# Kernel tuning notes

Measured on AMD Instinct MI355X. Metric: run time of the kernel, lower is better.

The kernel has to match this reference:

```python
import math
import jax, jax.numpy as jnp
from jax import lax
import numpy as np

B, T, D = 4, 8192, 1024
NUM_PATCHES = 512
EPS = 1e-6

def setup_inputs() -> dict:
    key = jax.random.key(0)
    ks = jax.random.split(key, 4)
    h = D // 2
    x = jax.random.normal(ks[0], (B, T, D), dtype=jnp.float32)
    conv1_w = jax.random.normal(ks[1], (h, D, 3), dtype=jnp.float32) * 0.02
    conv1_b = jnp.zeros((h,), jnp.float32)
    conv2_w = jax.random.normal(ks[2], (1, h, 3), dtype=jnp.float32) * 0.02
    conv2_b = jnp.zeros((1,), jnp.float32)
    norm_w = jnp.ones((D,), jnp.float32)
    return {"x": x, "conv1_w": conv1_w, "conv1_b": conv1_b,
            "conv2_w": conv2_w, "conv2_b": conv2_b, "norm_w": norm_w}

def _conv1d(x_ncw, w, b):
    y = lax.conv_general_dilated(x_ncw, w, window_strides=(1,), padding=[(1, 1)],
                                 dimension_numbers=("NCW", "OIW", "NCW"))
    return y + b[None, :, None]

def reference(x, conv1_w, conv1_b, conv2_w, conv2_b, norm_w):
    b, t, d = x.shape
    k = NUM_PATCHES
    seg = t // k  # T divisible by k, so all segments have equal length

    # LearnedBoundaryPredictor: conv -> gelu -> conv -> logits (B, T)
    xc = jnp.transpose(x, (0, 2, 1))  # (B, D, T)
    hcv = jax.nn.gelu(_conv1d(xc, conv1_w, conv1_b), approximate=False)
    logits = _conv1d(hcv, conv2_w, conv2_b)[:, 0, :]  # (B, T)

    # per-segment softmax-weighted centroid + normalized entropy (vectorized)
    seg_logits = logits.reshape(b, k, seg)
    w = jax.nn.softmax(seg_logits, axis=-1)                      # (B, k, seg)
    pos = jnp.arange(t, dtype=x.dtype).reshape(1, k, seg)
    boundaries = jnp.sum(w * pos, axis=-1)                        # (B, k)
    ent = -jnp.sum(w * jnp.log(jnp.clip(w, 1e-8)), axis=-1)
    entropy_signal = ent / jnp.asarray(math.log(max(seg, 2)), x.dtype)

    # gather byte embeddings at integer boundary positions
    idx = jnp.clip(boundaries.astype(jnp.int32), 0, t - 1)       # (B, k)
    patches = jnp.take_along_axis(x, idx[:, :, None], axis=1)    # (B, k, D)

    # RMSNorm
    rms = lax.rsqrt(jnp.mean(patches * patches, axis=-1, keepdims=True) + EPS)
    out = patches * rms * norm_w
    return out, entropy_signal
```

## Files before the change

kernel.cpp:

```cpp
#include <hip/hip_runtime.h>
#include <hip/hip_bf16.h>
#include <math.h>

#define T_LEN 8192
#define D_DIM 1024
#define H_DIM 512
#define NPATCH 512
#define SEG 16

typedef _Float16 f16;
typedef _Float16 f16x4 __attribute__((ext_vector_type(4)));
typedef _Float16 f16x8 __attribute__((ext_vector_type(8)));
typedef float f32x4 __attribute__((ext_vector_type(4)));

#define BMR 256
#define BNR 128
#define NBM2 128
#define NBN2 4
#define QL2 258
#define PADT (T_LEN + 2)
#define RSCALE 2048.0f
#define RINV   4.8828125e-4f

#define BUFB 49152
#define NSTEP 96

__device__ __forceinline__ void gll16(const void* g, void* l) {
    __builtin_amdgcn_global_load_lds((const __attribute__((address_space(1))) void*)g,
                                     (__attribute__((address_space(3))) void*)l, 16, 0, 0);
}

__global__ __launch_bounds__(256) void k_split_x(const float* __restrict__ x,
                                                 f16* __restrict__ xh, f16* __restrict__ xls) {
    size_t i4 = (size_t)blockIdx.x * 256 + threadIdx.x;
    size_t e = i4 * 4;
    int d = (int)(e % D_DIM);
    size_t row = e / D_DIM;
    int pt = (int)(row % PADT);
    int b = (int)(row / PADT);
    f16x4 h, lo;
    if (pt == 0 || pt == PADT - 1) {
        h = (f16x4){0, 0, 0, 0}; lo = (f16x4){0, 0, 0, 0};
    } else {
        float4 v = *(const float4*)(x + ((size_t)b * T_LEN + pt - 1) * D_DIM + d);
        f16 h0 = (f16)v.x, h1 = (f16)v.y, h2 = (f16)v.z, h3 = (f16)v.w;
        h = (f16x4){h0, h1, h2, h3};
        lo = (f16x4){(f16)((v.x - (float)h0) * RSCALE), (f16)((v.y - (float)h1) * RSCALE),
                     (f16)((v.z - (float)h2) * RSCALE), (f16)((v.w - (float)h3) * RSCALE)};
    }
    *(f16x4*)(xh + e) = h;
    *(f16x4*)(xls + e) = lo;
}

__global__ void k_split_w(const float* __restrict__ w1, f16* __restrict__ ws) {
    int idx = blockIdx.x * 256 + threadIdx.x;
    if (idx >= 3 * H_DIM * D_DIM) return;
    int i = idx % D_DIM;
    int o = (idx / D_DIM) % H_DIM;
    int j = idx / (D_DIM * H_DIM);
    float v = w1[((size_t)o * D_DIM + i) * 3 + j];
    f16 h = (f16)v;
    f16 l = (f16)((v - (float)h) * RSCALE);
    ws[((size_t)(j * 2 + 0) * H_DIM + o) * D_DIM + i] = h;
    ws[((size_t)(j * 2 + 1) * H_DIM + o) * D_DIM + i] = l;
}

#define MM3(mi, nj, AH, AL, BH, BL)                                                       \
    ahh[mi][nj] = __builtin_amdgcn_mfma_f32_16x16x32_f16(AH, BH, ahh[mi][nj], 0, 0, 0);   \
    axx[mi][nj] = __builtin_amdgcn_mfma_f32_16x16x32_f16(AH, BL, axx[mi][nj], 0, 0, 0);   \
    axx[mi][nj] = __builtin_amdgcn_mfma_f32_16x16x32_f16(AL, BH, axx[mi][nj], 0, 0, 0);

__global__ __launch_bounds__(512, 2) void k_conv_gemm_f16(
    const f16* __restrict__ xh, const f16* __restrict__ xls,
    const f16* __restrict__ wsd, const float* __restrict__ b1,
    const float* __restrict__ w2, float* __restrict__ partials)
{
    __shared__ __align__(16) char smem[3 * BUFB + 6144];
    const int tid = threadIdx.x;
    const int l = tid & 63, wv = tid >> 6;
    const int wr = wv >> 1, wc = wv & 1;

    int bid = blockIdx.x;
    int logical = (bid & 7) * 64 + (bid >> 3);
    const int bm = logical >> 2, bn = logical & 3;
    const int batch = bm >> 5;
    const int lt0 = (bm & 31) * BMR;
    const int n0 = bn * BNR;

    f32x4 ahh[4][4], axx[4][4];
    #pragma unroll
    for (int mi = 0; mi < 4; ++mi)
        #pragma unroll
        for (int nj = 0; nj < 4; ++nj) {
            ahh[mi][nj] = (f32x4){0.f, 0.f, 0.f, 0.f};
            axx[mi][nj] = (f32x4){0.f, 0.f, 0.f, 0.f};
        }

    const int kb = l >> 4, c15 = l & 15;

    const f16* base0[6];
    int jstr[6];
    #pragma unroll
    for (int u = 0; u < 6; ++u) {
        int s = wv * 6 + u;
        if (s < 32) {
            int which = s >> 4, sl = s & 15;
            int m = sl * 16 + (l >> 2);
            int ch = (l & 3) ^ ((m >> 1) & 3);
            base0[u] = (which ? xls : xh) + ((size_t)batch * PADT + lt0) * D_DIM
                       + (size_t)m * D_DIM + ch * 8;
            jstr[u] = D_DIM;
        } else {
            int s2 = s - 32, which = s2 >> 3, sl = s2 & 7;
            int n = sl * 16 + (l >> 2);
            int ch = (l & 3) ^ ((n >> 1) & 3);
            base0[u] = wsd + ((size_t)which * H_DIM + n0) * D_DIM + (size_t)n * D_DIM + ch * 8;
            jstr[u] = 2 * H_DIM * D_DIM;
        }
    }

    int aoff_[4], boff_[4];
    #pragma unroll
    for (int mi = 0; mi < 4; ++mi) {
        int m = wr * 64 + mi * 16 + c15;
        aoff_[mi] = m * 64 + ((kb ^ ((m >> 1) & 3)) * 16);
    }
    #pragma unroll
    for (int nj = 0; nj < 4; ++nj) {
        int n = wc * 64 + nj * 16 + c15;
        boff_[nj] = n * 64 + ((kb ^ ((n >> 1) & 3)) * 16);
    }

    #pragma unroll
    for (int u = 0; u < 6; ++u)
        gll16(base0[u], smem + (wv * 6 + u) * 1024);
    #pragma unroll
    for (int u = 0; u < 6; ++u)
        gll16(base0[u] + 32, smem + BUFB + (wv * 6 + u) * 1024);
    asm volatile("s_waitcnt vmcnt(6)" ::: "memory");
    __builtin_amdgcn_s_barrier();

    for (int t = 0; t < NSTEP; ++t) {
        char* buf = smem + (t % 3) * BUFB;
        f16x8 ah0, al0, ah1, al1, ah2, al2, ah3, al3;
        f16x8 bh0, bl0, bh1, bl1, bh2, bl2, bh3, bl3;

        ah0 = *(const f16x8*)(buf + aoff_[0]);          al0 = *(const f16x8*)(buf + 16384 + aoff_[0]);
        ah1 = *(const f16x8*)(buf + aoff_[1]);          al1 = *(const f16x8*)(buf + 16384 + aoff_[1]);
        ah2 = *(const f16x8*)(buf + aoff_[2]);          al2 = *(const f16x8*)(buf + 16384 + aoff_[2]);
        ah3 = *(const f16x8*)(buf + aoff_[3]);          al3 = *(const f16x8*)(buf + 16384 + aoff_[3]);
        bh0 = *(const f16x8*)(buf + 32768 + boff_[0]);  bl0 = *(const f16x8*)(buf + 40960 + boff_[0]);
        bh1 = *(const f16x8*)(buf + 32768 + boff_[1]);  bl1 = *(const f16x8*)(buf + 40960 + boff_[1]);
        bh2 = *(const f16x8*)(buf + 32768 + boff_[2]);  bl2 = *(const f16x8*)(buf + 40960 + boff_[2]);
        bh3 = *(const f16x8*)(buf + 32768 + boff_[3]);  bl3 = *(const f16x8*)(buf + 40960 + boff_[3]);

        {
            int sv = t + 2;
            if (sv < NSTEP) {
                char* dsty = smem + (sv % 3) * BUFB;
                int jj = sv >> 5, ko = (sv & 31) * 32;
                #pragma unroll
                for (int u = 0; u < 6; ++u)
                    gll16(base0[u] + (size_t)jj * jstr[u] + ko, dsty + (wv * 6 + u) * 1024);
            }
        }

        __builtin_amdgcn_s_setprio(1);
        MM3(0, 0, ah0, al0, bh0, bl0); MM3(0, 1, ah0, al0, bh1, bl1);
        MM3(1, 0, ah1, al1, bh0, bl0); MM3(1, 1, ah1, al1, bh1, bl1);
        MM3(2, 0, ah2, al2, bh0, bl0); MM3(2, 1, ah2, al2, bh1, bl1);
        MM3(3, 0, ah3, al3, bh0, bl0); MM3(3, 1, ah3, al3, bh1, bl1);
        MM3(2, 2, ah2, al2, bh2, bl2); MM3(2, 3, ah2, al2, bh3, bl3);
        MM3(3, 2, ah3, al3, bh2, bl2); MM3(3, 3, ah3, al3, bh3, bl3);
        MM3(0, 2, ah0, al0, bh2, bl2); MM3(0, 3, ah0, al0, bh3, bl3);
        MM3(1, 2, ah1, al1, bh2, bl2); MM3(1, 3, ah1, al1, bh3, bl3);
        __builtin_amdgcn_s_setprio(0);

        if (t < NSTEP - 2)
            asm volatile("s_waitcnt vmcnt(6)" ::: "memory");
        else if (t == NSTEP - 2)
            asm volatile("s_waitcnt vmcnt(0)" ::: "memory");
        __builtin_amdgcn_s_barrier();
    }

    float* lp_lds = (float*)(smem + 3 * BUFB);
    #pragma unroll
    for (int mi = 0; mi < 4; ++mi) {
        float lp[4][3] = {};
        #pragma unroll
        for (int nj = 0; nj < 4; ++nj) {
            int n = n0 + wc * 64 + nj * 16 + c15;
            float bias = b1[n];
            float w2m1 = w2[n * 3 + 2];
            float w20  = w2[n * 3 + 1];
            float w2p1 = w2[n * 3 + 0];
            #pragma unroll
            for (int r = 0; r < 4; ++r) {
                float v = ahh[mi][nj][r] + axx[mi][nj][r] * RINV + bias;
                float g = 0.5f * v * (1.f + erff(v * 0.70710678118654752f));
                lp[r][0] = fmaf(g, w2m1, lp[r][0]);
                lp[r][1] = fmaf(g, w20,  lp[r][1]);
                lp[r][2] = fmaf(g, w2p1, lp[r][2]);
            }
        }
        #pragma unroll
        for (int r = 0; r < 4; ++r)
            #pragma unroll
            for (int d = 0; d < 3; ++d) {
                float v = lp[r][d];
                v += __shfl_xor(v, 1, 64);
                v += __shfl_xor(v, 2, 64);
                v += __shfl_xor(v, 4, 64);
                v += __shfl_xor(v, 8, 64);
                lp[r][d] = v;
            }
        if (c15 == 0) {
            int m = wr * 64 + mi * 16 + kb * 4;
            #pragma unroll
            for (int r = 0; r < 4; ++r)
                #pragma unroll
                for (int d = 0; d < 3; ++d)
                    lp_lds[(wc * 3 + d) * 256 + m + r] = lp[r][d];
        }
    }
    __syncthreads();

    float* pout = partials + (size_t)(bm * NBN2 + bn) * QL2;
    for (int q = tid; q < QL2; q += 512) {
        int tloc = lt0 + q - 1;
        if (tloc >= 0 && tloc < T_LEN) {
            float v = 0.f;
            #pragma unroll
            for (int w2c = 0; w2c < 2; ++w2c) {
                if (q >= 1 && q <= 256) v += lp_lds[(w2c * 3 + 1) * 256 + q - 1];
                if (q >= 2)             v += lp_lds[(w2c * 3 + 2) * 256 + q - 2];
                if (q < 256)            v += lp_lds[(w2c * 3 + 0) * 256 + q];
            }
            pout[q] = v;
        }
    }
}

__global__ void k_reduce2(const float* __restrict__ partials,
                          const float* __restrict__ b2, float* __restrict__ logits) {
    int M = blockIdx.x * 256 + threadIdx.x;
    if (M >= 4 * T_LEN) return;
    int t = M & (T_LEN - 1);
    int bm = M >> 8;
    int mq = M & 255;
    int q = mq + 1;
    float s = b2[0];
    #pragma unroll
    for (int bn = 0; bn < NBN2; ++bn)
        s += partials[(size_t)(bm * NBN2 + bn) * QL2 + q];
    if (mq == 0 && t != 0) {
        #pragma unroll
        for (int bn = 0; bn < NBN2; ++bn)
            s += partials[(size_t)((bm - 1) * NBN2 + bn) * QL2 + (QL2 - 1)];
    }
    if (mq == 255 && t != T_LEN - 1) {
        #pragma unroll
        for (int bn = 0; bn < NBN2; ++bn)
            s += partials[(size_t)((bm + 1) * NBN2 + bn) * QL2 + 0];
    }
    logits[M] = s;
}

__global__ __launch_bounds__(256) void k_finalize(
    const float* __restrict__ x, const float* __restrict__ logits,
    const float* __restrict__ norm_w, float* __restrict__ out)
{
    int blk = blockIdx.x;
    int b = blk >> 9, p = blk & 511;
    const float* lg = logits + b * T_LEN + p * SEG;

    float l[SEG];
    #pragma unroll
    for (int i = 0; i < SEG; ++i) l[i] = lg[i];
    float mx = l[0];
    #pragma unroll
    for (int i = 1; i < SEG; ++i) mx = fmaxf(mx, l[i]);
    float w[SEG];
    float s = 0.f;
    #pragma unroll
    for (int i = 0; i < SEG; ++i) { w[i] = expf(l[i] - mx); s += w[i]; }
    float inv = 1.f / s;
    float boundary = 0.f, ent = 0.f;
    #pragma unroll
    for (int i = 0; i < SEG; ++i) {
        float wi = w[i] * inv;
        boundary += wi * (float)(p * SEG + i);
        ent -= wi * logf(fmaxf(wi, 1e-8f));
    }
    ent *= 0.36067376022224085f;

    int idx = (int)boundary;
    idx = min(max(idx, 0), T_LEN - 1);

    const float* row = x + ((size_t)b * T_LEN + idx) * D_DIM;
    int tid = threadIdx.x;
    float v[4];
    float ss = 0.f;
    #pragma unroll
    for (int r = 0; r < 4; ++r) {
        int c = tid + r * 256;
        v[r] = row[c];
        ss = fmaf(v[r], v[r], ss);
    }
    #pragma unroll
    for (int off = 32; off > 0; off >>= 1) ss += __shfl_down(ss, off, 64);
    __shared__ float sred[4];
    if ((tid & 63) == 0) sred[tid >> 6] = ss;
    __syncthreads();
    float tot = sred[0] + sred[1] + sred[2] + sred[3];
    float rms = rsqrtf(tot * (1.f / 1024.f) + 1e-6f);

    float* o0 = out + ((size_t)b * NPATCH + p) * D_DIM;
    #pragma unroll
    for (int r = 0; r < 4; ++r) {
        int c = tid + r * 256;
        o0[c] = v[r] * rms * norm_w[c];
    }
    if (tid == 0)
        out[(size_t)4 * NPATCH * D_DIM + b * NPATCH + p] = ent;
}

#define BM 128
#define BN 128
#define BK 16
#define NBM (4 * T_LEN / BM)
#define NBN (H_DIM / BN)
#define QLEN 130

__global__ void k_transpose_w1(const float* __restrict__ w1, float* __restrict__ w1t) {
    int idx = blockIdx.x * 256 + threadIdx.x;
    if (idx >= 3 * D_DIM * H_DIM) return;
    int o = idx % H_DIM;
    int i = (idx / H_DIM) % D_DIM;
    int j = idx / (H_DIM * D_DIM);
    w1t[idx] = w1[(o * D_DIM + i) * 3 + j];
}

__global__ __launch_bounds__(256) void k_conv_gemm(
    const float* __restrict__ x, const float* __restrict__ w1t,
    const float* __restrict__ b1, const float* __restrict__ w2,
    float* __restrict__ partials)
{
    __shared__ float As[BK][BM + 4];
    __shared__ float Bs[BK][BN];
    __shared__ float ld_lp[3][BM];

    const int bm = blockIdx.x, bn = blockIdx.y;
    const int m0 = bm * BM;
    const int batch = m0 / T_LEN;
    const int t0 = m0 % T_LEN;
    const int n0 = bn * BN;
    const int tid = threadIdx.x;
    const int tx = tid & 15, ty = tid >> 4;

    float acc[8][8] = {};

    const int a_col = (tid & 3) * 4;
    const int a_row = tid >> 2;
    const int b_row = tid >> 5;
    const int b_col = (tid & 31) * 4;

    const float* xb = x + (size_t)batch * T_LEN * D_DIM;

    for (int j = 0; j < 3; ++j) {
        const float* wj = w1t + (size_t)j * D_DIM * H_DIM;
        const int tshift = j - 1;
        for (int k0 = 0; k0 < D_DIM; k0 += BK) {
            #pragma unroll
            for (int rr = 0; rr < 2; ++rr) {
                int m = a_row + rr * 64;
                int tt = t0 + m + tshift;
                float4 v = make_float4(0.f, 0.f, 0.f, 0.f);
                if (tt >= 0 && tt < T_LEN)
                    v = *(const float4*)(xb + (size_t)tt * D_DIM + k0 + a_col);
                As[a_col + 0][m] = v.x; As[a_col + 1][m] = v.y;
                As[a_col + 2][m] = v.z; As[a_col + 3][m] = v.w;
            }
            #pragma unroll
            for (int rr = 0; rr < 2; ++rr) {
                int kk = b_row + rr * 8;
                *(float4*)&Bs[kk][b_col] =
                    *(const float4*)(wj + (size_t)(k0 + kk) * H_DIM + n0 + b_col);
            }
            __syncthreads();
            #pragma unroll
            for (int kk = 0; kk < BK; ++kk) {
                float a[8], bb[8];
                *(float4*)&a[0]  = *(const float4*)&As[kk][ty * 8];
                *(float4*)&a[4]  = *(const float4*)&As[kk][ty * 8 + 4];
                *(float4*)&bb[0] = *(const float4*)&Bs[kk][tx * 8];
                *(float4*)&bb[4] = *(const float4*)&Bs[kk][tx * 8 + 4];
                #pragma unroll
                for (int i = 0; i < 8; ++i) {
                    #pragma unroll
                    for (int ll = 0; ll < 8; ++ll)
                        acc[i][ll] = fmaf(a[i], bb[ll], acc[i][ll]);
                }
            }
            __syncthreads();
        }
    }

    float lp[8][3];
    #pragma unroll
    for (int i = 0; i < 8; ++i) { lp[i][0] = 0.f; lp[i][1] = 0.f; lp[i][2] = 0.f; }
    #pragma unroll
    for (int ll = 0; ll < 8; ++ll) {
        int n = n0 + tx * 8 + ll;
        float bias = b1[n];
        float w2m1 = w2[n * 3 + 2];
        float w20  = w2[n * 3 + 1];
        float w2p1 = w2[n * 3 + 0];
        #pragma unroll
        for (int i = 0; i < 8; ++i) {
            float v = acc[i][ll] + bias;
            float g = 0.5f * v * (1.f + erff(v * 0.70710678118654752f));
            lp[i][0] = fmaf(g, w2m1, lp[i][0]);
            lp[i][1] = fmaf(g, w20,  lp[i][1]);
            lp[i][2] = fmaf(g, w2p1, lp[i][2]);
        }
    }
    #pragma unroll
    for (int i = 0; i < 8; ++i) {
        #pragma unroll
        for (int d = 0; d < 3; ++d) {
            float v = lp[i][d];
            v += __shfl_xor(v, 1, 64);
            v += __shfl_xor(v, 2, 64);
            v += __shfl_xor(v, 4, 64);
            v += __shfl_xor(v, 8, 64);
            lp[i][d] = v;
        }
    }
    if (tx == 0) {
        #pragma unroll
        for (int i = 0; i < 8; ++i) {
            ld_lp[0][ty * 8 + i] = lp[i][0];
            ld_lp[1][ty * 8 + i] = lp[i][1];
            ld_lp[2][ty * 8 + i] = lp[i][2];
        }
    }
    __syncthreads();
    float* pout = partials + (size_t)(bm * NBN + bn) * QLEN;
    for (int q = tid; q < QLEN; q += 256) {
        int t = t0 + q - 1;
        if (t >= 0 && t < T_LEN) {
            float v = 0.f;
            if (q >= 1 && q <= BM) v += ld_lp[1][q - 1];
            if (q >= 2)            v += ld_lp[2][q - 2];
            if (q < BM)            v += ld_lp[0][q];
            pout[q] = v;
        }
    }
}

__global__ void k_reduce_logits(const float* __restrict__ partials,
                                const float* __restrict__ b2,
                                float* __restrict__ logits) {
    int M = blockIdx.x * 256 + threadIdx.x;
    if (M >= 4 * T_LEN) return;
    int t = M % T_LEN;
    int bm = M / BM;
    int q = (M % BM) + 1;
    float s = b2[0];
    #pragma unroll
    for (int bn = 0; bn < NBN; ++bn)
        s += partials[(size_t)(bm * NBN + bn) * QLEN + q];
    if ((M % BM) == 0 && t != 0) {
        #pragma unroll
        for (int bn = 0; bn < NBN; ++bn)
            s += partials[(size_t)((bm - 1) * NBN + bn) * QLEN + (QLEN - 1)];
    }
    if ((M % BM) == BM - 1 && t != T_LEN - 1) {
        #pragma unroll
        for (int bn = 0; bn < NBN; ++bn)
            s += partials[(size_t)((bm + 1) * NBN + bn) * QLEN + 0];
    }
    logits[M] = s;
}

extern "C" void kernel_launch(void* const* d_in, const int* in_sizes, int n_in,
                              void* d_out, int out_size, void* d_ws, size_t ws_size,
                              hipStream_t stream) {
    const float* x  = (const float*)d_in[0];
    const float* w1 = (const float*)d_in[1];
    const float* b1 = (const float*)d_in[2];
    const float* w2 = (const float*)d_in[3];
    const float* b2 = (const float*)d_in[4];
    const float* nw = (const float*)d_in[5];
    float* out = (float*)d_out;

    const size_t XS_ELEMS = (size_t)4 * PADT * D_DIM;
    const size_t WS_ELEMS = (size_t)3 * 2 * H_DIM * D_DIM;
    const size_t P2_FLOATS = (size_t)NBM2 * NBN2 * QL2;
    const size_t NEED = XS_ELEMS * 2 * sizeof(f16) + WS_ELEMS * sizeof(f16)
                      + (P2_FLOATS + 4 * T_LEN) * sizeof(float);

    if (ws_size >= NEED) {
        f16* xh = (f16*)d_ws;
        f16* xls = xh + XS_ELEMS;
        f16* wsd = xls + XS_ELEMS;
        float* partials = (float*)(wsd + WS_ELEMS);
        float* logits = partials + P2_FLOATS;

        k_split_x<<<(int)(XS_ELEMS / 4 / 256), 256, 0, stream>>>(x, xh, xls);
        k_split_w<<<(3 * H_DIM * D_DIM + 255) / 256, 256, 0, stream>>>(w1, wsd);
        k_conv_gemm_f16<<<NBM2 * NBN2, 512, 0, stream>>>(xh, xls, wsd, b1, w2, partials);
        k_reduce2<<<(4 * T_LEN + 255) / 256, 256, 0, stream>>>(partials, b2, logits);
        k_finalize<<<2048, 256, 0, stream>>>(x, logits, nw, out);
    } else {
        float* w1t      = (float*)d_ws;
        float* partials = w1t + 3 * D_DIM * H_DIM;
        float* logits   = partials + (size_t)NBM * NBN * QLEN;

        k_transpose_w1<<<(3 * D_DIM * H_DIM + 255) / 256, 256, 0, stream>>>(w1, w1t);
        k_conv_gemm<<<dim3(NBM, NBN), 256, 0, stream>>>(x, w1t, b1, w2, partials);
        k_reduce_logits<<<(4 * T_LEN + 255) / 256, 256, 0, stream>>>(partials, b2, logits);
        k_finalize<<<2048, 256, 0, stream>>>(x, logits, nw, out);
    }
}
```

Measured before the change: 337.6 us.

## Halve conv GEMM block to four waves with 128x64 per-wave tiles

The conv GEMM block shrinks from 8 to 4 waves while keeping the same 256x128 block tile. Each wave now computes a 128x64 sub-tile with twice the accumulators, so each LDS fragment read feeds more MFMAs. Global-to-LDS address generation now uses running pointers with a jump at each tap boundary, and the prefetch is issued before the LDS reads. The trade-off is much higher register pressure and only one wave per SIMD, which leaves less room to hide latency.

Result: slower. 1.339 ms (+296.5%).

```diff
diff --git a/kernel.cpp b/kernel.cpp
--- a/kernel.cpp
+++ b/kernel.cpp
@@ -24,6 +24,7 @@
 
 #define BUFB 49152
 #define NSTEP 96
+#define BBND  (2 * H_DIM * D_DIM * 2 - 31 * 64)
 
 __device__ __forceinline__ void gll16(const void* g, void* l) {
     __builtin_amdgcn_global_load_lds((const __attribute__((address_space(1))) void*)g,
@@ -70,7 +71,7 @@
     axx[mi][nj] = __builtin_amdgcn_mfma_f32_16x16x32_f16(AH, BL, axx[mi][nj], 0, 0, 0);   \
     axx[mi][nj] = __builtin_amdgcn_mfma_f32_16x16x32_f16(AL, BH, axx[mi][nj], 0, 0, 0);
 
-__global__ __launch_bounds__(512, 2) void k_conv_gemm_f16(
+__global__ __launch_bounds__(256, 1) void k_conv_gemm_f16(
     const f16* __restrict__ xh, const f16* __restrict__ xls,
     const f16* __restrict__ wsd, const float* __restrict__ b1,
     const float* __restrict__ w2, float* __restrict__ partials)
@@ -87,9 +88,9 @@
     const int lt0 = (bm & 31) * BMR;
     const int n0 = bn * BNR;
 
-    f32x4 ahh[4][4], axx[4][4];
-    #pragma unroll
-    for (int mi = 0; mi < 4; ++mi)
+    f32x4 ahh[8][4], axx[8][4];
+    #pragma unroll
+    for (int mi = 0; mi < 8; ++mi)
         #pragma unroll
         for (int nj = 0; nj < 4; ++nj) {
             ahh[mi][nj] = (f32x4){0.f, 0.f, 0.f, 0.f};
@@ -98,86 +99,109 @@
 
     const int kb = l >> 4, c15 = l & 15;
 
-    const f16* base0[6];
-    int jstr[6];
-    #pragma unroll
-    for (int u = 0; u < 6; ++u) {
-        int s = wv * 6 + u;
-        if (s < 32) {
-            int which = s >> 4, sl = s & 15;
+    const char* sp[12];
+    int bdel[12];
+    #pragma unroll
+    for (int u = 0; u < 12; ++u) {
+        int S = wv * 12 + u;
+        if (S < 32) {
+            int which = S >> 4, sl = S & 15;
             int m = sl * 16 + (l >> 2);
             int ch = (l & 3) ^ ((m >> 1) & 3);
-            base0[u] = (which ? xls : xh) + ((size_t)batch * PADT + lt0) * D_DIM
-                       + (size_t)m * D_DIM + ch * 8;
-            jstr[u] = D_DIM;
+            sp[u] = (const char*)((which ? xls : xh)
+                   + ((size_t)batch * PADT + lt0 + m) * D_DIM + ch * 8);
+            bdel[u] = 64;
         } else {
-            int s2 = s - 32, which = s2 >> 3, sl = s2 & 7;
+            int s2 = S - 32, which = s2 >> 3, sl = s2 & 7;
             int n = sl * 16 + (l >> 2);
             int ch = (l & 3) ^ ((n >> 1) & 3);
-            base0[u] = wsd + ((size_t)which * H_DIM + n0) * D_DIM + (size_t)n * D_DIM + ch * 8;
-            jstr[u] = 2 * H_DIM * D_DIM;
-        }
-    }
-
-    int aoff_[4], boff_[4];
-    #pragma unroll
-    for (int mi = 0; mi < 4; ++mi) {
-        int m = wr * 64 + mi * 16 + c15;
-        aoff_[mi] = m * 64 + ((kb ^ ((m >> 1) & 3)) * 16);
+            sp[u] = (const char*)(wsd + ((size_t)which * H_DIM + n0) * D_DIM
+                   + (size_t)n * D_DIM + ch * 8);
+            bdel[u] = BBND;
+        }
+    }
+
+    int aoffL[8], boffL[4];
+    #pragma unroll
+    for (int mi = 0; mi < 8; ++mi) {
+        int m = wr * 128 + mi * 16 + c15;
+        aoffL[mi] = m * 64 + ((kb ^ ((m >> 1) & 3)) * 16);
     }
     #pragma unroll
     for (int nj = 0; nj < 4; ++nj) {
         int n = wc * 64 + nj * 16 + c15;
-        boff_[nj] = n * 64 + ((kb ^ ((n >> 1) & 3)) * 16);
-    }
-
-    #pragma unroll
-    for (int u = 0; u < 6; ++u)
-        gll16(base0[u], smem + (wv * 6 + u) * 1024);
-    #pragma unroll
-    for (int u = 0; u < 6; ++u)
-        gll16(base0[u] + 32, smem + BUFB + (wv * 6 + u) * 1024);
-    asm volatile("s_waitcnt vmcnt(6)" ::: "memory");
+        boffL[nj] = n * 64 + ((kb ^ ((n >> 1) & 3)) * 16);
+    }
+
+    #pragma unroll
+    for (int u = 0; u < 12; ++u) {
+        gll16(sp[u], smem + (wv * 12 + u) * 1024);
+        sp[u] += 64;
+    }
+    #pragma unroll
+    for (int u = 0; u < 12; ++u) {
+        gll16(sp[u], smem + BUFB + (wv * 12 + u) * 1024);
+        sp[u] += 64;
+    }
+    asm volatile("s_waitcnt vmcnt(12)" ::: "memory");
     __builtin_amdgcn_s_barrier();
 
     for (int t = 0; t < NSTEP; ++t) {
         char* buf = smem + (t % 3) * BUFB;
-        f16x8 ah0, al0, ah1, al1, ah2, al2, ah3, al3;
+
+        if (t + 2 < NSTEP) {
+            char* dsty = smem + ((t + 2) % 3) * BUFB;
+            bool bnd = (((t + 3) & 31) == 0);
+            #pragma unroll
+            for (int u = 0; u < 12; ++u) {
+                gll16(sp[u], dsty + (wv * 12 + u) * 1024);
+                sp[u] += bnd ? bdel[u] : 64;
+            }
+        }
+
         f16x8 bh0, bl0, bh1, bl1, bh2, bl2, bh3, bl3;
-
-        ah0 = *(const f16x8*)(buf + aoff_[0]);          al0 = *(const f16x8*)(buf + 16384 + aoff_[0]);
-        ah1 = *(const f16x8*)(buf + aoff_[1]);          al1 = *(const f16x8*)(buf + 16384 + aoff_[1]);
-        ah2 = *(const f16x8*)(buf + aoff_[2]);          al2 = *(const f16x8*)(buf + 16384 + aoff_[2]);
-        ah3 = *(const f16x8*)(buf + aoff_[3]);          al3 = *(const f16x8*)(buf + 16384 + aoff_[3]);
-        bh0 = *(const f16x8*)(buf + 32768 + boff_[0]);  bl0 = *(const f16x8*)(buf + 40960 + boff_[0]);
-        bh1 = *(const f16x8*)(buf + 32768 + boff_[1]);  bl1 = *(const f16x8*)(buf + 40960 + boff_[1]);
-        bh2 = *(const f16x8*)(buf + 32768 + boff_[2]);  bl2 = *(const f16x8*)(buf + 40960 + boff_[2]);
-        bh3 = *(const f16x8*)(buf + 32768 + boff_[3]);  bl3 = *(const f16x8*)(buf + 40960 + boff_[3]);
+        bh0 = *(const f16x8*)(buf + 32768 + boffL[0]);  bl0 = *(const f16x8*)(buf + 40960 + boffL[0]);
+        bh1 = *(const f16x8*)(buf + 32768 + boffL[1]);  bl1 = *(const f16x8*)(buf + 40960 + boffL[1]);
+        bh2 = *(const f16x8*)(buf + 32768 + boffL[2]);  bl2 = *(const f16x8*)(buf + 40960 + boffL[2]);
+        bh3 = *(const f16x8*)(buf + 32768 + boffL[3]);  bl3 = *(const f16x8*)(buf + 40960 + boffL[3]);
 
         {
-            int sv = t + 2;
-            if (sv < NSTEP) {
-                char* dsty = smem + (sv % 3) * BUFB;
-                int jj = sv >> 5, ko = (sv & 31) * 32;
-                #pragma unroll
-                for (int u = 0; u < 6; ++u)
-                    gll16(base0[u] + (size_t)jj * jstr[u] + ko, dsty + (wv * 6 + u) * 1024);
-            }
-        }
-
-        __builtin_amdgcn_s_setprio(1);
-        MM3(0, 0, ah0, al0, bh0, bl0); MM3(0, 1, ah0, al0, bh1, bl1);
-        MM3(1, 0, ah1, al1, bh0, bl0); MM3(1, 1, ah1, al1, bh1, bl1);
-        MM3(2, 0, ah2, al2, bh0, bl0); MM3(2, 1, ah2, al2, bh1, bl1);
-        MM3(3, 0, ah3, al3, bh0, bl0); MM3(3, 1, ah3, al3, bh1, bl1);
-        MM3(2, 2, ah2, al2, bh2, bl2); MM3(2, 3, ah2, al2, bh3, bl3);
-        MM3(3, 2, ah3, al3, bh2, bl2); MM3(3, 3, ah3, al3, bh3, bl3);
-        MM3(0, 2, ah0, al0, bh2, bl2); MM3(0, 3, ah0, al0, bh3, bl3);
-        MM3(1, 2, ah1, al1, bh2, bl2); MM3(1, 3, ah1, al1, bh3, bl3);
-        __builtin_amdgcn_s_setprio(0);
+            f16x8 ah0, al0, ah1, al1, ah2, al2, ah3, al3;
+            ah0 = *(const f16x8*)(buf + aoffL[0]);  al0 = *(const f16x8*)(buf + 16384 + aoffL[0]);
+            ah1 = *(const f16x8*)(buf + aoffL[1]);  al1 = *(const f16x8*)(buf + 16384 + aoffL[1]);
+            ah2 = *(const f16x8*)(buf + aoffL[2]);  al2 = *(const f16x8*)(buf + 16384 + aoffL[2]);
+            ah3 = *(const f16x8*)(buf + aoffL[3]);  al3 = *(const f16x8*)(buf + 16384 + aoffL[3]);
+            __builtin_amdgcn_s_setprio(1);
+            MM3(0, 0, ah0, al0, bh0, bl0); MM3(0, 1, ah0, al0, bh1, bl1);
+            MM3(1, 0, ah1, al1, bh0, bl0); MM3(1, 1, ah1, al1, bh1, bl1);
+            MM3(2, 0, ah2, al2, bh0, bl0); MM3(2, 1, ah2, al2, bh1, bl1);
+            MM3(3, 0, ah3, al3, bh0, bl0); MM3(3, 1, ah3, al3, bh1, bl1);
+            MM3(0, 2, ah0, al0, bh2, bl2); MM3(0, 3, ah0, al0, bh3, bl3);
+            MM3(1, 2, ah1, al1, bh2, bl2); MM3(1, 3, ah1, al1, bh3, bl3);
+            MM3(2, 2, ah2, al2, bh2, bl2); MM3(2, 3, ah2, al2, bh3, bl3);
+            MM3(3, 2, ah3, al3, bh2, bl2); MM3(3, 3, ah3, al3, bh3, bl3);
+            __builtin_amdgcn_s_setprio(0);
+        }
+        {
+            f16x8 ah4, al4, ah5, al5, ah6, al6, ah7, al7;
+            ah4 = *(const f16x8*)(buf + aoffL[4]);  al4 = *(const f16x8*)(buf + 16384 + aoffL[4]);
+            ah5 = *(const f16x8*)(buf + aoffL[5]);  al5 = *(const f16x8*)(buf + 16384 + aoffL[5]);
+            ah6 = *(const f16x8*)(buf + aoffL[6]);  al6 = *(const f16x8*)(buf + 16384 + aoffL[6]);
+            ah7 = *(const f16x8*)(buf + aoffL[7]);  al7 = *(const f16x8*)(buf + 16384 + aoffL[7]);
+            __builtin_amdgcn_s_setprio(1);
+            MM3(4, 0, ah4, al4, bh0, bl0); MM3(4, 1, ah4, al4, bh1, bl1);
+            MM3(5, 0, ah5, al5, bh0, bl0); MM3(5, 1, ah5, al5, bh1, bl1);
+            MM3(6, 0, ah6, al6, bh0, bl0); MM3(6, 1, ah6, al6, bh1, bl1);
+            MM3(7, 0, ah7, al7, bh0, bl0); MM3(7, 1, ah7, al7, bh1, bl1);
+            MM3(4, 2, ah4, al4, bh2, bl2); MM3(4, 3, ah4, al4, bh3, bl3);
+            MM3(5, 2, ah5, al5, bh2, bl2); MM3(5, 3, ah5, al5, bh3, bl3);
+            MM3(6, 2, ah6, al6, bh2, bl2); MM3(6, 3, ah6, al6, bh3, bl3);
+            MM3(7, 2, ah7, al7, bh2, bl2); MM3(7, 3, ah7, al7, bh3, bl3);
+            __builtin_amdgcn_s_setprio(0);
+        }
 
         if (t < NSTEP - 2)
-            asm volatile("s_waitcnt vmcnt(6)" ::: "memory");
+            asm volatile("s_waitcnt vmcnt(12)" ::: "memory");
         else if (t == NSTEP - 2)
             asm volatile("s_waitcnt vmcnt(0)" ::: "memory");
         __builtin_amdgcn_s_barrier();
@@ -185,7 +209,7 @@
 
     float* lp_lds = (float*)(smem + 3 * BUFB);
     #pragma unroll
-    for (int mi = 0; mi < 4; ++mi) {
+    for (int mi = 0; mi < 8; ++mi) {
         float lp[4][3] = {};
         #pragma unroll
         for (int nj = 0; nj < 4; ++nj) {
@@ -215,7 +239,7 @@
                 lp[r][d] = v;
             }
         if (c15 == 0) {
-            int m = wr * 64 + mi * 16 + kb * 4;
+            int m = wr * 128 + mi * 16 + kb * 4;
             #pragma unroll
             for (int r = 0; r < 4; ++r)
                 #pragma unroll
@@ -226,7 +250,7 @@
     __syncthreads();
 
     float* pout = partials + (size_t)(bm * NBN2 + bn) * QL2;
-    for (int q = tid; q < QL2; q += 512) {
+    for (int q = tid; q < QL2; q += 256) {
         int tloc = lt0 + q - 1;
         if (tloc >= 0 && tloc < T_LEN) {
             float v = 0.f;
@@ -510,7 +534,7 @@
 
         k_split_x<<<(int)(XS_ELEMS / 4 / 256), 256, 0, stream>>>(x, xh, xls);
         k_split_w<<<(3 * H_DIM * D_DIM + 255) / 256, 256, 0, stream>>>(w1, wsd);
-        k_conv_gemm_f16<<<NBM2 * NBN2, 512, 0, stream>>>(xh, xls, wsd, b1, w2, partials);
+        k_conv_gemm_f16<<<NBM2 * NBN2, 256, 0, stream>>>(xh, xls, wsd, b1, w2, partials);
         k_reduce2<<<(4 * T_LEN + 255) / 256, 256, 0, stream>>>(partials, b2, logits);
         k_finalize<<<2048, 256, 0, stream>>>(x, logits, nw, out);
     } else {
```
